# Performance work log

Measured on AMD Instinct MI355X. Metric: run time of the kernel, lower is better.

The kernel has to match this reference:

```python
import jax, jax.numpy as jnp
import numpy as np

NB_HEAD = 16
DIM_PER_HEAD = 64
EMB = 1024
B, SQ, SK = 4, 2048, 2048


def setup_inputs() -> dict:
    key = jax.random.key(0)
    ks = jax.random.split(key, 8)
    scale = 1.0 / np.sqrt(EMB)
    return {
        "hidden_state_query": jax.random.normal(ks[0], (B, SQ, EMB), jnp.float32),
        "hidden_state_key": jax.random.normal(ks[1], (B, SK, EMB), jnp.float32),
        "hidden_state_value": jax.random.normal(ks[2], (B, SK, EMB), jnp.float32),
        "attention_mask": jax.random.randint(ks[3], (B, SQ, SK), 0, 2).astype(bool),
        "Wq": jax.random.uniform(ks[4], (NB_HEAD * DIM_PER_HEAD, EMB), jnp.float32, -scale, scale),
        "Wk": jax.random.uniform(ks[5], (NB_HEAD * DIM_PER_HEAD, EMB), jnp.float32, -scale, scale),
        "Wv": jax.random.uniform(ks[6], (NB_HEAD * DIM_PER_HEAD, EMB), jnp.float32, -scale, scale),
        "Wo": jax.random.uniform(ks[7], (EMB, NB_HEAD * DIM_PER_HEAD), jnp.float32, -scale, scale),
    }


def reference(hidden_state_query, hidden_state_key, hidden_state_value,
              attention_mask, Wq, Wk, Wv, Wo):
    bs, sq, _ = hidden_state_query.shape
    sk = hidden_state_key.shape[1]
    # projections (nn.Linear without bias: x @ W.T)
    q = (hidden_state_query @ Wq.T).reshape(bs, sq, NB_HEAD, DIM_PER_HEAD).transpose(0, 2, 1, 3)
    k = (hidden_state_key @ Wk.T).reshape(bs, sk, NB_HEAD, DIM_PER_HEAD).transpose(0, 2, 1, 3)
    v = (hidden_state_value @ Wv.T).reshape(bs, sk, NB_HEAD, DIM_PER_HEAD).transpose(0, 2, 1, 3)
    scores = jnp.einsum('bhqd,bhkd->bhqk', q, k) / jnp.sqrt(jnp.asarray(DIM_PER_HEAD, q.dtype))
    attn = jax.nn.softmax(scores, axis=-1)
    # POST-softmax zero masking (True -> 0), broadcast over heads; no renormalization
    attn = jnp.where(attention_mask[:, None, :, :], jnp.asarray(0.0, attn.dtype), attn)
    ctx = jnp.einsum('bhqk,bhkd->bhqd', attn, v)  # [B,H,Sq,Dh]
    ctx = ctx.transpose(0, 2, 1, 3).reshape(bs, sq, NB_HEAD * DIM_PER_HEAD)
    return ctx @ Wo.T + hidden_state_query
```

## Files before the change

### kernel.cpp

```cpp
#include <hip/hip_runtime.h>
#include <hip/hip_bf16.h>
#include <stdint.h>

typedef __bf16 bf16_t;
typedef bf16_t bf16x2 __attribute__((ext_vector_type(2)));
typedef bf16_t bf16x8 __attribute__((ext_vector_type(8)));
typedef float  f32x4  __attribute__((ext_vector_type(4)));
typedef float  f32x16 __attribute__((ext_vector_type(16)));
typedef unsigned uint2v __attribute__((ext_vector_type(2)));

#define NB_HEAD 16
#define DH      64
#define EMB     1024
#define BATCH   4
#define SEQ     2048
#define NTOK    (BATCH*SEQ)

#define QSCALE 0.1803368801111204f

__device__ __forceinline__ void gload_lds16(const void* g, void* l) {
  __builtin_amdgcn_global_load_lds(
      (const __attribute__((address_space(1))) void*)g,
      (__attribute__((address_space(3))) void*)l, 16, 0, 0);
}

__device__ __forceinline__ uint32_t pkbf(float a, float b) {
  bf16x2 v = { (bf16_t)a, (bf16_t)b };
  return __builtin_bit_cast(uint32_t, v);
}

__device__ __forceinline__ void cvt8_body(const float* __restrict__ in,
                                          bf16_t* __restrict__ out, int i) {
  const float4* p = reinterpret_cast<const float4*>(in) + (size_t)i * 2;
  float4 a = p[0], b = p[1];
  uint4 r;
  r.x = pkbf(a.x, a.y); r.y = pkbf(a.z, a.w);
  r.z = pkbf(b.x, b.y); r.w = pkbf(b.z, b.w);
  reinterpret_cast<uint4*>(out)[i] = r;
}

__device__ __forceinline__ void mkand_body(const uint8_t* __restrict__ m,
                                           uint16_t* __restrict__ out, int i) {
  uint2 v = reinterpret_cast<const uint2*>(m)[i];
  uint4 r;
  uint32_t lo = v.x, hi = v.y;
  uint16_t e[8];
#pragma unroll
  for (int j = 0; j < 4; j++) e[j]     = (uint16_t)(((lo >> (8 * j)) & 0xFF) - 1);
#pragma unroll
  for (int j = 0; j < 4; j++) e[4 + j] = (uint16_t)(((hi >> (8 * j)) & 0xFF) - 1);
  r.x = (uint32_t)e[0] | ((uint32_t)e[1] << 16);
  r.y = (uint32_t)e[2] | ((uint32_t)e[3] << 16);
  r.z = (uint32_t)e[4] | ((uint32_t)e[5] << 16);
  r.w = (uint32_t)e[6] | ((uint32_t)e[7] << 16);
  reinterpret_cast<uint4*>(out)[i] = r;
}

__global__ void __launch_bounds__(256)
prep(const float* __restrict__ hq, const float* __restrict__ hk,
     const float* __restrict__ hv, const float* __restrict__ Wq,
     const float* __restrict__ Wk, const float* __restrict__ Wv,
     const float* __restrict__ Wo,
     bf16_t* hq_b, bf16_t* hk_b, bf16_t* hv_b,
     bf16_t* Wq_b, bf16_t* Wk_b, bf16_t* Wv_b, bf16_t* Wo_b,
     const uint8_t* __restrict__ mask, uint16_t* __restrict__ mand) {
  const int bid = blockIdx.x;
  if (bid < 12288) {
    const int seg = bid >> 12;
    const float* src = seg == 0 ? hq : seg == 1 ? hk : hv;
    bf16_t*      dst = seg == 0 ? hq_b : seg == 1 ? hk_b : hv_b;
    cvt8_body(src, dst, (bid & 4095) * 256 + (int)threadIdx.x);
  } else if (bid < 14336) {
    const int sb = bid - 12288;
    const int seg = sb >> 9;
    const float* src = seg == 0 ? Wq : seg == 1 ? Wk : seg == 2 ? Wv : Wo;
    bf16_t*      dst = seg == 0 ? Wq_b : seg == 1 ? Wk_b : seg == 2 ? Wv_b : Wo_b;
    cvt8_body(src, dst, (sb & 511) * 256 + (int)threadIdx.x);
  } else {
    mkand_body(mask, mand, (bid - 14336) * 256 + (int)threadIdx.x);
  }
}

__global__ void __launch_bounds__(256)
mkand(const uint8_t* __restrict__ m, uint16_t* __restrict__ out) {
  mkand_body(m, out, blockIdx.x * 256 + (int)threadIdx.x);
}

#define BM 128
#define BN 128
#define BKT 64

template<int EPI>
__global__ void __launch_bounds__(256, 2)
gemm_bt(const bf16_t* __restrict__ A, const bf16_t* __restrict__ Bw,
        bf16_t* __restrict__ Cb, float* __restrict__ Cf,
        const float* __restrict__ resid, float qscale) {
  __shared__ bf16_t As[2][BM * BKT];
  __shared__ bf16_t Bs[2][BN * BKT];
  const int K = EMB, N = EMB;
  const int t    = threadIdx.x;
  const int lane = t & 63, w = t >> 6;
  const int wr = w >> 1, wc = w & 1;
  const int l15 = lane & 15, l4 = lane >> 4;

  const int lin = blockIdx.x + 8 * blockIdx.y;
  const int nl  = (lin & 7) * 64 + (lin >> 3);
  const int rowBase = (nl >> 3) * BM, colBase = (nl & 7) * BN;

  f32x4 acc[4][4];
#pragma unroll
  for (int i = 0; i < 4; i++)
#pragma unroll
    for (int j = 0; j < 4; j++) acc[i][j] = f32x4{0.f, 0.f, 0.f, 0.f};

  const int lin16 = w * 1024 + lane * 16;

#pragma unroll
  for (int i = 0; i < 4; ++i) {
    int off  = i * 4096 + lin16;
    int row  = off >> 7, colb = off & 127;
    gload_lds16((const char*)A  + (((size_t)(rowBase + row)) * K) * 2 + colb, (char*)As[0] + off);
    gload_lds16((const char*)Bw + (((size_t)(colBase + row)) * K) * 2 + colb, (char*)Bs[0] + off);
  }
  __syncthreads();

  int cur = 0;
  for (int k0 = 0; k0 < K; k0 += BKT) {
    if (k0 + BKT < K) {
      const int nb = cur ^ 1;
#pragma unroll
      for (int i = 0; i < 4; ++i) {
        int off  = i * 4096 + lin16;
        int row  = off >> 7, colb = off & 127;
        gload_lds16((const char*)A  + (((size_t)(rowBase + row)) * K + k0 + BKT) * 2 + colb, (char*)As[nb] + off);
        gload_lds16((const char*)Bw + (((size_t)(colBase + row)) * K + k0 + BKT) * 2 + colb, (char*)Bs[nb] + off);
      }
    }
#pragma unroll
    for (int kc = 0; kc < 2; ++kc) {
      bf16x8 af[4], bfb[4];
#pragma unroll
      for (int mi = 0; mi < 4; mi++)
        af[mi] = *reinterpret_cast<const bf16x8*>(
            &As[cur][(wr * 64 + mi * 16 + l15) * BKT + kc * 32 + l4 * 8]);
#pragma unroll
      for (int ni = 0; ni < 4; ni++)
        bfb[ni] = *reinterpret_cast<const bf16x8*>(
            &Bs[cur][(wc * 64 + ni * 16 + l15) * BKT + kc * 32 + l4 * 8]);
      __builtin_amdgcn_s_setprio(1);
#pragma unroll
      for (int mi = 0; mi < 4; mi++)
#pragma unroll
        for (int ni = 0; ni < 4; ni++)
          acc[mi][ni] = __builtin_amdgcn_mfma_f32_16x16x32_bf16(
              af[mi], bfb[ni], acc[mi][ni], 0, 0, 0);
      __builtin_amdgcn_s_setprio(0);
    }
    __syncthreads();
    cur ^= 1;
  }

#pragma unroll
  for (int mi = 0; mi < 4; mi++) {
#pragma unroll
    for (int ni = 0; ni < 4; ni++) {
      const int m0 = rowBase + wr * 64 + mi * 16 + l4 * 4;
      const int n  = colBase + wc * 64 + ni * 16 + l15;
      if (EPI == 1) {
        size_t base = ((size_t)((m0 >> 11) * 1024 + n)) * 2048 + (m0 & 2047);
        uint2 st;
        st.x = pkbf(acc[mi][ni][0], acc[mi][ni][1]);
        st.y = pkbf(acc[mi][ni][2], acc[mi][ni][3]);
        *reinterpret_cast<uint2*>(Cb + base) = st;
      } else {
#pragma unroll
        for (int r = 0; r < 4; r++) {
          int m = m0 + r;
          float v = acc[mi][ni][r];
          if (EPI == 0) {
            Cb[(size_t)m * N + n] = (bf16_t)(v * qscale);
          } else if (EPI == 3) {
            Cb[(((size_t)((m >> 11) * 16 + (n >> 6))) * 2048 + (m & 2047)) * 64 + (n & 63)] = (bf16_t)v;
          } else {
            Cf[(size_t)m * N + n] = v + resid[(size_t)m * N + n];
          }
        }
      }
    }
  }
}

__global__ void __launch_bounds__(512, 2)
attn32(const bf16_t* __restrict__ Qb, const bf16_t* __restrict__ Kh,
       const bf16_t* __restrict__ Vt, const uint16_t* __restrict__ Mand,
       bf16_t* __restrict__ ctx) {
  __shared__ __align__(16) bf16_t Ks[2][64 * 64];
  __shared__ __align__(16) bf16_t Vs[2][64 * 64];

  const int t = threadIdx.x, lane = t & 63, wid = t >> 6;
  const int q = lane & 31, hi = lane >> 5;

  const int lin = blockIdx.x + 8 * (blockIdx.y + 16 * blockIdx.z);
  const int nl  = (lin & 7) * 64 + (lin >> 3);
  const int bx = nl & 7, h = (nl >> 3) & 15, b = nl >> 7;

  const int q0 = bx * 256 + wid * 32;
  const int qrow = b * SEQ + q0 + q;

  const int srow  = t >> 3;
  const int scolx = ((t & 7) ^ ((t >> 3) & 7)) * 16;
  const char* kg = (const char*)(Kh + ((size_t)(b * NB_HEAD + h)) * SEQ * DH);
  const char* vg = (const char*)(Vt + ((size_t)(b * NB_HEAD + h)) * DH * SEQ);

  const bf16_t* qp = Qb + (size_t)qrow * EMB + h * DH + hi * 8;
  bf16x8 qf[4];
#pragma unroll
  for (int d = 0; d < 4; d++) qf[d] = *reinterpret_cast<const bf16x8*>(qp + d * 16);

  f32x16 o0 = {0}, o1 = {0};
  float lrun = 0.f;
  const uint16_t* mbase = Mand + (size_t)qrow * SEQ;
  const int qx = (q & 7) << 4;

  gload_lds16(kg + (size_t)srow * 128 + scolx,  (char*)Ks[0] + t * 16);
  gload_lds16(vg + (size_t)srow * 4096 + scolx, (char*)Vs[0] + t * 16);
  __syncthreads();

  int cur = 0;
  for (int kb = 0; kb < SEQ; kb += 64) {
    if (kb + 64 < SEQ) {
      const int nb = cur ^ 1;
      gload_lds16(kg + (size_t)(kb + 64) * 128 + (size_t)srow * 128 + scolx,
                  (char*)Ks[nb] + t * 16);
      gload_lds16(vg + (size_t)(kb + 64) * 2 + (size_t)srow * 4096 + scolx,
                  (char*)Vs[nb] + t * 16);
    }

    const char* kls = (const char*)Ks[cur];
    f32x16 p0 = {0}, p1 = {0};
    __builtin_amdgcn_s_setprio(1);
#pragma unroll
    for (int dsl = 0; dsl < 4; dsl++) {
      const int cb = (dsl * 32 + hi * 16) ^ qx;
      bf16x8 kf0 = *reinterpret_cast<const bf16x8*>(kls + q * 128 + cb);
      bf16x8 kf1 = *reinterpret_cast<const bf16x8*>(kls + (32 + q) * 128 + cb);
      p0 = __builtin_amdgcn_mfma_f32_32x32x16_bf16(kf0, qf[dsl], p0, 0, 0, 0);
      p1 = __builtin_amdgcn_mfma_f32_32x32x16_bf16(kf1, qf[dsl], p1, 0, 0, 0);
    }
    __builtin_amdgcn_s_setprio(0);

    uint4 mv[4];
#pragma unroll
    for (int ks = 0; ks < 4; ks++)
      mv[ks] = *reinterpret_cast<const uint4*>(mbase + kb + 16 * ks + 8 * hi);

    float ps = 0.f;
#pragma unroll
    for (int i = 0; i < 16; i++) { p0[i] = __builtin_amdgcn_exp2f(p0[i]); ps += p0[i]; }
#pragma unroll
    for (int i = 0; i < 16; i++) { p1[i] = __builtin_amdgcn_exp2f(p1[i]); ps += p1[i]; }
    ps += __shfl_xor(ps, 32);
    lrun += ps;

    const char* vls = (const char*)Vs[cur];
#pragma unroll
    for (int ks = 0; ks < 4; ks++) {
      const int s8 = (ks & 1) * 8;
      float e0, e1, e2, e3, e4, e5, e6, e7;
      if (ks < 2) {
        e0 = p0[s8+0]; e1 = p0[s8+1]; e2 = p0[s8+2]; e3 = p0[s8+3];
        e4 = p0[s8+4]; e5 = p0[s8+5]; e6 = p0[s8+6]; e7 = p0[s8+7];
      } else {
        e0 = p1[s8+0]; e1 = p1[s8+1]; e2 = p1[s8+2]; e3 = p1[s8+3];
        e4 = p1[s8+4]; e5 = p1[s8+5]; e6 = p1[s8+6]; e7 = p1[s8+7];
      }
      uint32_t a0 = pkbf(e0, e1), a1 = pkbf(e2, e3);
      uint32_t a2 = pkbf(e4, e5), a3 = pkbf(e6, e7);
      uint2v s02 = __builtin_amdgcn_permlane32_swap(a0, a2, false, false);
      uint2v s13 = __builtin_amdgcn_permlane32_swap(a1, a3, false, false);
      uint4 fr;
      fr.x = s02[0]; fr.y = s13[0]; fr.z = s02[1]; fr.w = s13[1];
      fr.x &= mv[ks].x; fr.y &= mv[ks].y; fr.z &= mv[ks].z; fr.w &= mv[ks].w;
      bf16x8 pa = __builtin_bit_cast(bf16x8, fr);
      const int cb = (ks * 32 + hi * 16) ^ qx;
      bf16x8 vf0 = *reinterpret_cast<const bf16x8*>(vls + q * 128 + cb);
      bf16x8 vf1 = *reinterpret_cast<const bf16x8*>(vls + (32 + q) * 128 + cb);
      __builtin_amdgcn_s_setprio(1);
      o0 = __builtin_amdgcn_mfma_f32_32x32x16_bf16(vf0, pa, o0, 0, 0, 0);
      o1 = __builtin_amdgcn_mfma_f32_32x32x16_bf16(vf1, pa, o1, 0, 0, 0);
      __builtin_amdgcn_s_setprio(0);
    }

    __syncthreads();
    cur ^= 1;
  }

  float inv = 1.0f / lrun;
  bf16_t* cp = ctx + (size_t)qrow * EMB + h * DH;
#pragma unroll
  for (int g = 0; g < 4; g++) {
    uint2 st;
    st.x = pkbf(o0[4*g+0] * inv, o0[4*g+1] * inv);
    st.y = pkbf(o0[4*g+2] * inv, o0[4*g+3] * inv);
    *reinterpret_cast<uint2*>(cp + 8 * g + 4 * hi) = st;
    st.x = pkbf(o1[4*g+0] * inv, o1[4*g+1] * inv);
    st.y = pkbf(o1[4*g+2] * inv, o1[4*g+3] * inv);
    *reinterpret_cast<uint2*>(cp + 32 + 8 * g + 4 * hi) = st;
  }
}

extern "C" void kernel_launch(void* const* d_in, const int* in_sizes, int n_in,
                              void* d_out, int out_size, void* d_ws, size_t ws_size,
                              hipStream_t stream) {
  const float*   hq   = (const float*)d_in[0];
  const float*   hk   = (const float*)d_in[1];
  const float*   hv   = (const float*)d_in[2];
  const uint8_t* mask = (const uint8_t*)d_in[3];
  const float*   Wq   = (const float*)d_in[4];
  const float*   Wk   = (const float*)d_in[5];
  const float*   Wv   = (const float*)d_in[6];
  const float*   Wo   = (const float*)d_in[7];
  float* out = (float*)d_out;

  char* ws = (char*)d_ws;
  const size_t SZ_H = (size_t)NTOK * EMB * 2;
  const size_t SZ_W = (size_t)EMB * EMB * 2;
  bf16_t* hq_b = (bf16_t*)(ws + 0 * SZ_H);
  bf16_t* hk_b = (bf16_t*)(ws + 1 * SZ_H);
  bf16_t* hv_b = (bf16_t*)(ws + 2 * SZ_H);
  bf16_t* Qb   = (bf16_t*)(ws + 3 * SZ_H);
  bf16_t* Kh   = (bf16_t*)(ws + 4 * SZ_H);
  bf16_t* Vt   = (bf16_t*)(ws + 5 * SZ_H);
  bf16_t* ctx  = (bf16_t*)(ws + 6 * SZ_H);
  bf16_t* Wq_b = (bf16_t*)(ws + 7 * SZ_H + 0 * SZ_W);
  bf16_t* Wk_b = (bf16_t*)(ws + 7 * SZ_H + 1 * SZ_W);
  bf16_t* Wv_b = (bf16_t*)(ws + 7 * SZ_H + 2 * SZ_W);
  bf16_t* Wo_b = (bf16_t*)(ws + 7 * SZ_H + 3 * SZ_W);

  const size_t MAND_OFF = 7 * SZ_H + 4 * SZ_W;
  const size_t MAND_SZ  = (size_t)BATCH * SEQ * SEQ * 2;
  const bool bigws = ws_size >= MAND_OFF + MAND_SZ;
  uint16_t* Mand = bigws ? (uint16_t*)(ws + MAND_OFF) : (uint16_t*)ws;

  prep<<<bigws ? 22528 : 14336, 256, 0, stream>>>(
      hq, hk, hv, Wq, Wk, Wv, Wo,
      hq_b, hk_b, hv_b, Wq_b, Wk_b, Wv_b, Wo_b, mask, Mand);

  dim3 ggrid(EMB / BN, NTOK / BM);
  gemm_bt<0><<<ggrid, 256, 0, stream>>>(hq_b, Wq_b, Qb, nullptr, nullptr, QSCALE);
  gemm_bt<3><<<ggrid, 256, 0, stream>>>(hk_b, Wk_b, Kh, nullptr, nullptr, 1.0f);
  gemm_bt<1><<<ggrid, 256, 0, stream>>>(hv_b, Wv_b, Vt, nullptr, nullptr, 1.0f);

  if (!bigws) mkand<<<8192, 256, 0, stream>>>(mask, Mand);

  attn32<<<dim3(SEQ / 256, NB_HEAD, BATCH), 512, 0, stream>>>(Qb, Kh, Vt, Mand, ctx);

  gemm_bt<2><<<ggrid, 256, 0, stream>>>(ctx, Wo_b, nullptr, out, hq, 1.0f);
}
```

Measured before the change: 241.8 us.

## Pre-tile K and V projections into MFMA fragment order for contiguous attention loads

The K and V projection epilogues now write into per-head 64-row blocks laid out in the exact order the attention MFMA fragments consume. The attention kernel then loads each 8KB tile with contiguous global-to-LDS copies and reads fragments at lane*16 offsets, dropping the XOR swizzle and strided V^T rows. The aim is to cut address arithmetic and get fully coalesced global loads and conflict-free LDS reads. The trade-off is more scattered 16-bit stores in the EPI==3 projection epilogue.

```diff
diff --git a/kernel.cpp b/kernel.cpp
--- a/kernel.cpp
+++ b/kernel.cpp
@@ -167,11 +167,13 @@
       const int m0 = rowBase + wr * 64 + mi * 16 + l4 * 4;
       const int n  = colBase + wc * 64 + ni * 16 + l15;
       if (EPI == 1) {
-        size_t base = ((size_t)((m0 >> 11) * 1024 + n)) * 2048 + (m0 & 2047);
+        const int bq = m0 >> 11, s0 = m0 & 2047, hh = n >> 6, d = n & 63;
+        size_t local = (size_t)(s0 >> 6) * 4096 + ((s0 >> 4) & 3) * 1024 +
+                       (d >> 5) * 512 + ((s0 >> 3) & 1) * 256 + (d & 31) * 8 + (s0 & 7);
         uint2 st;
         st.x = pkbf(acc[mi][ni][0], acc[mi][ni][1]);
         st.y = pkbf(acc[mi][ni][2], acc[mi][ni][3]);
-        *reinterpret_cast<uint2*>(Cb + base) = st;
+        *reinterpret_cast<uint2*>(Cb + (size_t)(bq * 16 + hh) * 131072 + local) = st;
       } else {
 #pragma unroll
         for (int r = 0; r < 4; r++) {
@@ -180,7 +182,10 @@
           if (EPI == 0) {
             Cb[(size_t)m * N + n] = (bf16_t)(v * qscale);
           } else if (EPI == 3) {
-            Cb[(((size_t)((m >> 11) * 16 + (n >> 6))) * 2048 + (m & 2047)) * 64 + (n & 63)] = (bf16_t)v;
+            const int bq = m >> 11, s = m & 2047, hh = n >> 6, d = n & 63;
+            size_t local = (size_t)(s >> 6) * 4096 + ((s >> 5) & 1) * 2048 +
+                           (d >> 4) * 512 + ((d >> 3) & 1) * 256 + (s & 31) * 8 + (d & 7);
+            Cb[(size_t)(bq * 16 + hh) * 131072 + local] = (bf16_t)v;
           } else {
             Cf[(size_t)m * N + n] = v + resid[(size_t)m * N + n];
           }
@@ -199,6 +204,7 @@
 
   const int t = threadIdx.x, lane = t & 63, wid = t >> 6;
   const int q = lane & 31, hi = lane >> 5;
+  const int l16 = lane * 16;
 
   const int lin = blockIdx.x + 8 * (blockIdx.y + 16 * blockIdx.z);
   const int nl  = (lin & 7) * 64 + (lin >> 3);
@@ -207,10 +213,8 @@
   const int q0 = bx * 256 + wid * 32;
   const int qrow = b * SEQ + q0 + q;
 
-  const int srow  = t >> 3;
-  const int scolx = ((t & 7) ^ ((t >> 3) & 7)) * 16;
   const char* kg = (const char*)(Kh + ((size_t)(b * NB_HEAD + h)) * SEQ * DH);
-  const char* vg = (const char*)(Vt + ((size_t)(b * NB_HEAD + h)) * DH * SEQ);
+  const char* vg = (const char*)(Vt + ((size_t)(b * NB_HEAD + h)) * SEQ * DH);
 
   const bf16_t* qp = Qb + (size_t)qrow * EMB + h * DH + hi * 8;
   bf16x8 qf[4];
@@ -220,20 +224,17 @@
   f32x16 o0 = {0}, o1 = {0};
   float lrun = 0.f;
   const uint16_t* mbase = Mand + (size_t)qrow * SEQ;
-  const int qx = (q & 7) << 4;
-
-  gload_lds16(kg + (size_t)srow * 128 + scolx,  (char*)Ks[0] + t * 16);
-  gload_lds16(vg + (size_t)srow * 4096 + scolx, (char*)Vs[0] + t * 16);
+
+  gload_lds16(kg + t * 16, (char*)Ks[0] + t * 16);
+  gload_lds16(vg + t * 16, (char*)Vs[0] + t * 16);
   __syncthreads();
 
   int cur = 0;
   for (int kb = 0; kb < SEQ; kb += 64) {
     if (kb + 64 < SEQ) {
       const int nb = cur ^ 1;
-      gload_lds16(kg + (size_t)(kb + 64) * 128 + (size_t)srow * 128 + scolx,
-                  (char*)Ks[nb] + t * 16);
-      gload_lds16(vg + (size_t)(kb + 64) * 2 + (size_t)srow * 4096 + scolx,
-                  (char*)Vs[nb] + t * 16);
+      gload_lds16(kg + (size_t)(kb + 64) * 128 + t * 16, (char*)Ks[nb] + t * 16);
+      gload_lds16(vg + (size_t)(kb + 64) * 128 + t * 16, (char*)Vs[nb] + t * 16);
     }
 
     const char* kls = (const char*)Ks[cur];
@@ -241,9 +242,8 @@
     __builtin_amdgcn_s_setprio(1);
 #pragma unroll
     for (int dsl = 0; dsl < 4; dsl++) {
-      const int cb = (dsl * 32 + hi * 16) ^ qx;
-      bf16x8 kf0 = *reinterpret_cast<const bf16x8*>(kls + q * 128 + cb);
-      bf16x8 kf1 = *reinterpret_cast<const bf16x8*>(kls + (32 + q) * 128 + cb);
+      bf16x8 kf0 = *reinterpret_cast<const bf16x8*>(kls + dsl * 1024 + l16);
+      bf16x8 kf1 = *reinterpret_cast<const bf16x8*>(kls + 4096 + dsl * 1024 + l16);
       p0 = __builtin_amdgcn_mfma_f32_32x32x16_bf16(kf0, qf[dsl], p0, 0, 0, 0);
       p1 = __builtin_amdgcn_mfma_f32_32x32x16_bf16(kf1, qf[dsl], p1, 0, 0, 0);
     }
@@ -282,9 +282,8 @@
       fr.x = s02[0]; fr.y = s13[0]; fr.z = s02[1]; fr.w = s13[1];
       fr.x &= mv[ks].x; fr.y &= mv[ks].y; fr.z &= mv[ks].z; fr.w &= mv[ks].w;
       bf16x8 pa = __builtin_bit_cast(bf16x8, fr);
-      const int cb = (ks * 32 + hi * 16) ^ qx;
-      bf16x8 vf0 = *reinterpret_cast<const bf16x8*>(vls + q * 128 + cb);
-      bf16x8 vf1 = *reinterpret_cast<const bf16x8*>(vls + (32 + q) * 128 + cb);
+      bf16x8 vf0 = *reinterpret_cast<const bf16x8*>(vls + ks * 2048 + l16);
+      bf16x8 vf1 = *reinterpret_cast<const bf16x8*>(vls + ks * 2048 + 1024 + l16);
       __builtin_amdgcn_s_setprio(1);
       o0 = __builtin_amdgcn_mfma_f32_32x32x16_bf16(vf0, pa, o0, 0, 0, 0);
       o1 = __builtin_amdgcn_mfma_f32_32x32x16_bf16(vf1, pa, o1, 0, 0, 0);
```

After: 244.6 us. About the same (+1.2%).
